# Kernel tuning notes

Hardware: AMD Instinct MI355X
Metric: run time of the kernel (lower is better)

The kernel has to match this reference:

```python
import jax, jax.numpy as jnp
import numpy as np

B, C, H, W = 4, 256, 64, 64
DQK = C // 8  # 32


def setup_inputs() -> dict:
    key = jax.random.key(0)
    ks = jax.random.split(key, 8)
    s = 0.02
    return {
        "x": jax.random.normal(ks[0], (B, C, H, W), dtype=jnp.float32),
        "Wq": jax.random.normal(ks[1], (DQK, C), dtype=jnp.float32) * s,
        "bq": jnp.zeros((DQK,), dtype=jnp.float32),
        "Wk": jax.random.normal(ks[2], (DQK, C), dtype=jnp.float32) * s,
        "bk": jnp.zeros((DQK,), dtype=jnp.float32),
        "Wv": jax.random.normal(ks[3], (C, C), dtype=jnp.float32) * s,
        "bv": jnp.zeros((C,), dtype=jnp.float32),
        "gamma": jax.random.normal(ks[4], (1,), dtype=jnp.float32) * 0.1,
    }


def reference(x, Wq, bq, Wk, bk, Wv, bv, gamma):
    b, c, h, w = x.shape
    n = h * w
    xf = x.reshape(b, c, n)  # [B, C, N]
    # 1x1 convs == per-pixel linear projections
    q = jnp.einsum('dc,bcn->bdn', Wq, xf) + bq[None, :, None]  # [B, C/8, N]
    k = jnp.einsum('dc,bcn->bdn', Wk, xf) + bk[None, :, None]  # [B, C/8, N]
    v = jnp.einsum('dc,bcn->bdn', Wv, xf) + bv[None, :, None]  # [B, C, N]
    # attn[b, i, j] = softmax_j( q_i . k_j / sqrt(C) )
    scores = jnp.einsum('bdn,bdm->bnm', q, k) / (c ** 0.5)  # [B, N, N]
    attn = jax.nn.softmax(scores, axis=-1)
    # out = v @ attn^T : out[b, c, i] = sum_j v[b, c, j] * attn[b, i, j]
    out = jnp.einsum('bcj,bij->bci', v, attn)  # [B, C, N]
    return (gamma * out + xf).reshape(b, c, h, w)
```

## Files before the change

kernel.cpp:

```cpp
#include <hip/hip_runtime.h>

#define NN 4096
#define CC 256
#define DQ 32
#define NB 4

typedef float        f32x4  __attribute__((ext_vector_type(4)));
typedef float        f32x16 __attribute__((ext_vector_type(16)));
typedef short        s16x4  __attribute__((ext_vector_type(4)));
typedef short        s16x8  __attribute__((ext_vector_type(8)));
typedef unsigned int u32x2  __attribute__((ext_vector_type(2)));
typedef unsigned int u32x4  __attribute__((ext_vector_type(4)));

__device__ __forceinline__ unsigned short f2bf(float f) {
  unsigned u = __builtin_bit_cast(unsigned, f);
  u += 0x7fffu + ((u >> 16) & 1u);
  return (unsigned short)(u >> 16);
}

__device__ __forceinline__ f32x4 mfma16(s16x4 a, s16x4 b, f32x4 c) {
  return __builtin_amdgcn_mfma_f32_16x16x16bf16_1k(a, b, c, 0, 0, 0);
}
__device__ __forceinline__ f32x16 mfma32b(s16x8 a, s16x8 b, f32x16 c) {
  return __builtin_amdgcn_mfma_f32_32x32x16_bf16(a, b, c, 0, 0, 0);
}

__device__ __forceinline__ s16x4 lo4(u32x4 r) { u32x2 t = {r[0], r[1]}; return __builtin_bit_cast(s16x4, t); }
__device__ __forceinline__ s16x4 hi4(u32x4 r) { u32x2 t = {r[2], r[3]}; return __builtin_bit_cast(s16x4, t); }
__device__ __forceinline__ s16x8 bc8(u32x4 r) { return __builtin_bit_cast(s16x8, r); }

__device__ __forceinline__ float fexp2(float x) {
  float r;
  asm("v_exp_f32 %0, %1" : "=v"(r) : "v"(x));
  return r;
}

#define XLS 264

__global__ __launch_bounds__(256)
void proj_kernel(const float* __restrict__ x,
                 const float* __restrict__ Wq, const float* __restrict__ bq,
                 const float* __restrict__ Wk, const float* __restrict__ bk,
                 const float* __restrict__ Wv, const float* __restrict__ bv,
                 unsigned short* __restrict__ QT,
                 unsigned short* __restrict__ KT,
                 unsigned short* __restrict__ Vm) {
  __shared__ unsigned short Xl[64 * XLS];
  const int tid = threadIdx.x;
  const int b   = blockIdx.y;
  const int n0  = blockIdx.x * 64;

  {
    const int n4 = (tid & 15) * 4;
    int c = tid >> 4;
    const float* xp = x + (size_t)(b * CC + c) * NN + n0 + n4;
    #pragma unroll
    for (int it = 0; it < 16; ++it) {
      f32x4 v = *reinterpret_cast<const f32x4*>(xp);
      #pragma unroll
      for (int e = 0; e < 4; ++e)
        Xl[(n4 + e) * XLS + c] = f2bf(v[e]);
      c += 16; xp += (size_t)16 * NN;
    }
  }
  __syncthreads();

  const int wave = tid >> 6;
  const int lane = tid & 63;
  const int l16  = lane & 15;
  const int g    = lane >> 4;
  const float qscale = 0.0901684400555602f;

  const float* wrowp[5];
  float wsc[5];
  #pragma unroll
  for (int rt = 0; rt < 5; ++rt) {
    const int R0 = (wave * 5 + rt) * 16;
    const int R  = R0 + l16;
    if (R0 < 32)      { wrowp[rt] = Wq + R * CC;        wsc[rt] = qscale; }
    else if (R0 < 64) { wrowp[rt] = Wk + (R - 32) * CC; wsc[rt] = 1.0f; }
    else              { wrowp[rt] = Wv + (R - 64) * CC; wsc[rt] = 1.0f; }
  }

  f32x4 acc[5][4];
  #pragma unroll
  for (int rt = 0; rt < 5; ++rt)
    #pragma unroll
    for (int nt = 0; nt < 4; ++nt) acc[rt][nt] = (f32x4){0.f, 0.f, 0.f, 0.f};

  for (int k0 = 0; k0 < CC; k0 += 32) {
    s16x4 xb[4][2];
    #pragma unroll
    for (int nt = 0; nt < 4; ++nt) {
      const unsigned short* p = &Xl[(l16 + 16 * nt) * XLS + k0 + 8 * g];
      u32x4 raw = *reinterpret_cast<const u32x4*>(p);
      xb[nt][0] = lo4(raw);
      xb[nt][1] = hi4(raw);
    }
    #pragma unroll
    for (int rt = 0; rt < 5; ++rt) {
      const float* wp = wrowp[rt] + k0 + 8 * g;
      f32x4 w0 = *reinterpret_cast<const f32x4*>(wp);
      f32x4 w1 = *reinterpret_cast<const f32x4*>(wp + 4);
      const float sc = wsc[rt];
      s16x4 wa0, wa1;
      #pragma unroll
      for (int e = 0; e < 4; ++e) {
        wa0[e] = (short)f2bf(w0[e] * sc);
        wa1[e] = (short)f2bf(w1[e] * sc);
      }
      #pragma unroll
      for (int nt = 0; nt < 4; ++nt) {
        acc[rt][nt] = mfma16(wa0, xb[nt][0], acc[rt][nt]);
        acc[rt][nt] = mfma16(wa1, xb[nt][1], acc[rt][nt]);
      }
    }
  }

  #pragma unroll
  for (int rt = 0; rt < 5; ++rt) {
    const int R0 = (wave * 5 + rt) * 16;
    float bias_r[4];
    {
      const float* bp; float bsc;
      if (R0 < 32)      { bp = bq + R0;      bsc = qscale; }
      else if (R0 < 64) { bp = bk + R0 - 32; bsc = 1.0f; }
      else              { bp = bv + R0 - 64; bsc = 1.0f; }
      #pragma unroll
      for (int r = 0; r < 4; ++r) bias_r[r] = bp[4 * g + r] * bsc;
    }
    #pragma unroll
    for (int nt = 0; nt < 4; ++nt) {
      const int n = n0 + nt * 16 + l16;
      float v0 = acc[rt][nt][0] + bias_r[0];
      float v1 = acc[rt][nt][1] + bias_r[1];
      float v2 = acc[rt][nt][2] + bias_r[2];
      float v3 = acc[rt][nt][3] + bias_r[3];
      if (R0 < 32) {
        u32x2 pk = { (unsigned)f2bf(v0) | ((unsigned)f2bf(v1) << 16),
                     (unsigned)f2bf(v2) | ((unsigned)f2bf(v3) << 16) };
        unsigned short* dst = QT + ((size_t)b * NN + n) * DQ + R0 + 4 * g;
        *reinterpret_cast<u32x2*>(dst) = pk;
      } else if (R0 < 64) {
        const int d0     = R0 - 32 + 4 * g;
        const int kh     = d0 >> 4;
        const int g2v    = (d0 >> 3) & 1;
        const int e0     = d0 & 7;
        const int jt     = n >> 5;
        const int lane_t = (n & 31) + 32 * g2v;
        u32x2 pk = { (unsigned)f2bf(v0) | ((unsigned)f2bf(v1) << 16),
                     (unsigned)f2bf(v2) | ((unsigned)f2bf(v3) << 16) };
        unsigned short* kd = KT + (((size_t)(b * 128 + jt) * 2 + kh) * 64 + lane_t) * 8 + e0;
        *reinterpret_cast<u32x2*>(kd) = pk;
      } else {
        const int c0  = R0 - 64 + 4 * g;
        const int cq  = c0 >> 5;
        const int cl  = c0 & 31;
        const int jt  = (n0 + nt * 16) >> 5;
        const int kh  = nt & 1;
        const int g2v = (l16 >> 2) & 1;
        const int e   = (l16 & 3) | (((l16 >> 3) & 1) << 2);
        unsigned short* vd = Vm
          + ((((size_t)(b * 128 + jt) * 8 + cq) * 2 + kh) * 64 + (cl + 32 * g2v)) * 8 + e;
        vd[0]  = f2bf(v0);
        vd[8]  = f2bf(v1);
        vd[16] = f2bf(v2);
        vd[24] = f2bf(v3);
      }
    }
  }
}


#define SM16(SS, L, P0_, P1_) { \
  const float p0=fexp2(SS[0]),  p1=fexp2(SS[1]),  p2=fexp2(SS[2]),  p3=fexp2(SS[3]); \
  const float p4=fexp2(SS[4]),  p5=fexp2(SS[5]),  p6=fexp2(SS[6]),  p7=fexp2(SS[7]); \
  const float p8=fexp2(SS[8]),  p9=fexp2(SS[9]),  pa=fexp2(SS[10]), pb=fexp2(SS[11]); \
  const float pc=fexp2(SS[12]), pd=fexp2(SS[13]), pe=fexp2(SS[14]), pf=fexp2(SS[15]); \
  L += (((p0+p1)+(p2+p3)) + ((p4+p5)+(p6+p7))) + (((p8+p9)+(pa+pb)) + ((pc+pd)+(pe+pf))); \
  unsigned q0,q1,q2,q3,q4,q5,q6,q7; \
  asm("v_cvt_pk_bf16_f32 %0, %1, %2" : "=v"(q0) : "v"(p0), "v"(p1)); \
  asm("v_cvt_pk_bf16_f32 %0, %1, %2" : "=v"(q1) : "v"(p2), "v"(p3)); \
  asm("v_cvt_pk_bf16_f32 %0, %1, %2" : "=v"(q2) : "v"(p4), "v"(p5)); \
  asm("v_cvt_pk_bf16_f32 %0, %1, %2" : "=v"(q3) : "v"(p6), "v"(p7)); \
  asm("v_cvt_pk_bf16_f32 %0, %1, %2" : "=v"(q4) : "v"(p8), "v"(p9)); \
  asm("v_cvt_pk_bf16_f32 %0, %1, %2" : "=v"(q5) : "v"(pa), "v"(pb)); \
  asm("v_cvt_pk_bf16_f32 %0, %1, %2" : "=v"(q6) : "v"(pc), "v"(pd)); \
  asm("v_cvt_pk_bf16_f32 %0, %1, %2" : "=v"(q7) : "v"(pe), "v"(pf)); \
  u32x4 _w0 = {q0,q1,q2,q3}, _w1 = {q4,q5,q6,q7}; \
  P0_ = bc8(_w0); P1_ = bc8(_w1); }

#define LOADK_IMPL(T, KA, KB) { \
  const int _tk = ((T) < 64) ? (T) : 63; \
  const size_t _o = (size_t)_tk * 1024; \
  KA = *(const u32x4*)(Kb + _o); \
  KB = *(const u32x4*)(Kb + _o + 512); }

#define LOADV_IMPL(T, V0, V1, V2, V3) { \
  const int _tv = ((T) < 64) ? (T) : 63; \
  const size_t _o = (size_t)_tv * 8192; \
  V0 = *(const u32x4*)(Vb + _o); \
  V1 = *(const u32x4*)(Vb + _o + 512); \
  V2 = *(const u32x4*)(Vb + _o + 1024); \
  V3 = *(const u32x4*)(Vb + _o + 1536); }

#define ITER_IMPL(T, KA, KB, V0, V1, V2, V3, NKA, NKB, NV0, NV1, NV2, NV3) { \
  LOADK_IMPL((T) + 1, NKA, NKB); \
  LOADV_IMPL((T) + 1, NV0, NV1, NV2, NV3); \
  f32x16 ss = mfma32b(bc8(KA), qf0, zz16); \
  ss = mfma32b(bc8(KB), qf1, ss); \
  s16x8 P0, P1; \
  SM16(ss, l, P0, P1); \
  o0 = mfma32b(bc8(V0), P0, o0); \
  o0 = mfma32b(bc8(V1), P1, o0); \
  o1 = mfma32b(bc8(V2), P0, o1); \
  o1 = mfma32b(bc8(V3), P1, o1); \
}
#define ITER(T, SETC, SETN) ITER_IMPL(T, SETC, SETN)

#define SET_A kA0, kB0, va0, va1, va2, va3
#define SET_B kA1, kB1, vb0, vb1, vb2, vb3

#define PUBLISH_CT(CT, OV) { \
  _Pragma("unroll") \
  for (int r = 0; r < 16; ++r) \
    fb[((cs * 2 + (CT)) * 16 + r) * 64 + lane] = OV[r]; }

#define FINAL_CT(CT, OV) { \
  _Pragma("unroll") \
  for (int r = 0; r < 16; ++r) { \
    const float oB = fb[((cs * 2 + (CT)) * 16 + r) * 64 + lane]; \
    const int   c  = cs * 64 + (CT) * 32 + (r & 3) + 8 * (r >> 2) + 4 * g2; \
    const size_t adr = ((size_t)b * CC + c) * NN + i; \
    out[adr] = ga * (OV[r] + oB) + x[adr]; } }

__global__ __launch_bounds__(512)
void attn_kernel(const unsigned short* __restrict__ QT,
                 const unsigned short* __restrict__ KT,
                 const unsigned short* __restrict__ Vm,
                 const float* __restrict__ x,
                 const float* __restrict__ gamma,
                 float* __restrict__ out) {
  __shared__ float fb[8192 + 32];

  const int tid  = threadIdx.x;
  const int wave = tid >> 6;
  const int jq   = wave >> 2;
  const int cs   = wave & 3;
  const int lane = tid & 63;
  const int l31  = lane & 31;
  const int g2   = lane >> 5;

  const int gid = blockIdx.x;
  const int rr  = gid & 7;
  const int qq  = gid >> 3;
  const int b   = rr >> 1;
  const int xt  = (qq << 1) | (rr & 1);
  const int ibase = xt * 32;
  const float gamma0 = gamma[0];

  const unsigned short* Qb = QT + ((size_t)b * NN + ibase + l31) * DQ;
  const s16x8 qf0 = bc8(*(const u32x4*)(Qb + 8 * g2));
  const s16x8 qf1 = bc8(*(const u32x4*)(Qb + 16 + 8 * g2));

  f32x16 o0, o1, zz16;
  #pragma unroll
  for (int r = 0; r < 16; ++r) { o0[r] = 0.f; o1[r] = 0.f; zz16[r] = 0.f; }
  float l = 0.f;

  const unsigned short* Kb = KT + (size_t)(b * 128 + jq * 64) * 1024 + lane * 8;
  const unsigned short* Vb = Vm + ((size_t)(b * 128 + jq * 64) * 8 + cs * 2) * 1024 + lane * 8;

  u32x4 kA0, kB0, va0, va1, va2, va3;
  u32x4 kA1, kB1, vb0, vb1, vb2, vb3;

  LOADK_IMPL(0, kA0, kB0);
  LOADV_IMPL(0, va0, va1, va2, va3);

  #pragma unroll 1
  for (int tt = 0; tt < 32; ++tt) {
    const int t = 2 * tt;
    ITER(t,     SET_A, SET_B);
    ITER(t + 1, SET_B, SET_A);
  }

  l += __shfl_xor(l, 32);

  if (jq == 1) {
    PUBLISH_CT(0, o0);
    PUBLISH_CT(1, o1);
    if (cs == 0 && g2 == 0) fb[8192 + l31] = l;
  }
  __syncthreads();
  if (jq == 0) {
    const float lB = fb[8192 + l31];
    const float ga = gamma0 / (l + lB);
    const int i = ibase + l31;
    FINAL_CT(0, o0);
    FINAL_CT(1, o1);
  }
}

extern "C" void kernel_launch(void* const* d_in, const int* in_sizes, int n_in,
                              void* d_out, int out_size, void* d_ws, size_t ws_size,
                              hipStream_t stream) {
  const float* x     = (const float*)d_in[0];
  const float* Wq    = (const float*)d_in[1];
  const float* bq    = (const float*)d_in[2];
  const float* Wk    = (const float*)d_in[3];
  const float* bk    = (const float*)d_in[4];
  const float* Wv    = (const float*)d_in[5];
  const float* bv    = (const float*)d_in[6];
  const float* gamma = (const float*)d_in[7];
  float* out = (float*)d_out;

  unsigned short* QT = (unsigned short*)d_ws;
  unsigned short* KT = QT + (size_t)NB * NN * DQ;
  unsigned short* Vm = KT + (size_t)NB * NN * DQ;

  dim3 gridP(64, NB), blkP(256);
  proj_kernel<<<gridP, blkP, 0, stream>>>(x, Wq, bq, Wk, bk, Wv, bv, QT, KT, Vm);
  attn_kernel<<<512, 512, 0, stream>>>(QT, KT, Vm, x, gamma, out);
}
```

Before: 86.21 us.

## Split key range four ways per block, widen channel slice per wave

Work inside each 512-thread block is repartitioned. Waves now split the key dimension into four quarters and the channel dimension into two halves of 128 channels, where before it was two key halves and four 64-channel slices. Each wave therefore recomputes fewer redundant QK scores and softmax exponentials (2 channel groups instead of 4 redo the same scores) while doing more PV MFMAs per score. In exchange each wave holds twice as many accumulator and V-prefetch registers, which may lower occupancy. The partial results go through a two-stage LDS reduction with an extra barrier, using 64KB of dynamic shared memory.

Result: no change. 85.02 us (-1.4%).

```diff
diff --git a/kernel.cpp b/kernel.cpp
--- a/kernel.cpp
+++ b/kernel.cpp
@@ -191,22 +191,27 @@
   P0_ = bc8(_w0); P1_ = bc8(_w1); }
 
 #define LOADK_IMPL(T, KA, KB) { \
-  const int _tk = ((T) < 64) ? (T) : 63; \
+  const int _tk = ((T) < 32) ? (T) : 31; \
   const size_t _o = (size_t)_tk * 1024; \
   KA = *(const u32x4*)(Kb + _o); \
   KB = *(const u32x4*)(Kb + _o + 512); }
 
-#define LOADV_IMPL(T, V0, V1, V2, V3) { \
-  const int _tv = ((T) < 64) ? (T) : 63; \
+#define LOADV_IMPL(T, V0, V1, V2, V3, V4, V5, V6, V7) { \
+  const int _tv = ((T) < 32) ? (T) : 31; \
   const size_t _o = (size_t)_tv * 8192; \
   V0 = *(const u32x4*)(Vb + _o); \
   V1 = *(const u32x4*)(Vb + _o + 512); \
   V2 = *(const u32x4*)(Vb + _o + 1024); \
-  V3 = *(const u32x4*)(Vb + _o + 1536); }
-
-#define ITER_IMPL(T, KA, KB, V0, V1, V2, V3, NKA, NKB, NV0, NV1, NV2, NV3) { \
+  V3 = *(const u32x4*)(Vb + _o + 1536); \
+  V4 = *(const u32x4*)(Vb + _o + 2048); \
+  V5 = *(const u32x4*)(Vb + _o + 2560); \
+  V6 = *(const u32x4*)(Vb + _o + 3072); \
+  V7 = *(const u32x4*)(Vb + _o + 3584); }
+
+#define ITER_IMPL(T, KA, KB, V0, V1, V2, V3, V4, V5, V6, V7, \
+                     NKA, NKB, NV0, NV1, NV2, NV3, NV4, NV5, NV6, NV7) { \
   LOADK_IMPL((T) + 1, NKA, NKB); \
-  LOADV_IMPL((T) + 1, NV0, NV1, NV2, NV3); \
+  LOADV_IMPL((T) + 1, NV0, NV1, NV2, NV3, NV4, NV5, NV6, NV7); \
   f32x16 ss = mfma32b(bc8(KA), qf0, zz16); \
   ss = mfma32b(bc8(KB), qf1, ss); \
   s16x8 P0, P1; \
@@ -215,22 +220,34 @@
   o0 = mfma32b(bc8(V1), P1, o0); \
   o1 = mfma32b(bc8(V2), P0, o1); \
   o1 = mfma32b(bc8(V3), P1, o1); \
+  o2 = mfma32b(bc8(V4), P0, o2); \
+  o2 = mfma32b(bc8(V5), P1, o2); \
+  o3 = mfma32b(bc8(V6), P0, o3); \
+  o3 = mfma32b(bc8(V7), P1, o3); \
 }
 #define ITER(T, SETC, SETN) ITER_IMPL(T, SETC, SETN)
 
-#define SET_A kA0, kB0, va0, va1, va2, va3
-#define SET_B kA1, kB1, vb0, vb1, vb2, vb3
-
-#define PUBLISH_CT(CT, OV) { \
+#define SET_A kA0, kB0, va0, va1, va2, va3, va4, va5, va6, va7
+#define SET_B kA1, kB1, vb0, vb1, vb2, vb3, vb4, vb5, vb6, vb7
+
+#define S1IDX(CT, R) ((((jq * 2 + cs) * 4 + (CT)) * 16 + (R)) * 64 + lane)
+#define S2IDX(CT, R) (((cs * 4 + (CT)) * 16 + (R)) * 64 + lane)
+#define LOFF 16384
+
+#define PUB1_CT(CT, OV) { \
   _Pragma("unroll") \
-  for (int r = 0; r < 16; ++r) \
-    fb[((cs * 2 + (CT)) * 16 + r) * 64 + lane] = OV[r]; }
-
-#define FINAL_CT(CT, OV) { \
+  for (int r = 0; r < 16; ++r) fb[S1IDX(CT, r)] = OV[r]; }
+#define ABS1_CT(CT, OV) { \
+  _Pragma("unroll") \
+  for (int r = 0; r < 16; ++r) OV[r] += fb[S1IDX(CT, r)]; }
+#define PUB2_CT(CT, OV) { \
+  _Pragma("unroll") \
+  for (int r = 0; r < 16; ++r) fb[S2IDX(CT, r)] = OV[r]; }
+#define FIN_CT(CT, OV) { \
   _Pragma("unroll") \
   for (int r = 0; r < 16; ++r) { \
-    const float oB = fb[((cs * 2 + (CT)) * 16 + r) * 64 + lane]; \
-    const int   c  = cs * 64 + (CT) * 32 + (r & 3) + 8 * (r >> 2) + 4 * g2; \
+    const float oB = fb[S2IDX(CT, r)]; \
+    const int   c  = cs * 128 + (CT) * 32 + (r & 3) + 8 * (r >> 2) + 4 * g2; \
     const size_t adr = ((size_t)b * CC + c) * NN + i; \
     out[adr] = ga * (OV[r] + oB) + x[adr]; } }
 
@@ -241,15 +258,17 @@
                  const float* __restrict__ x,
                  const float* __restrict__ gamma,
                  float* __restrict__ out) {
-  __shared__ float fb[8192 + 32];
+  extern __shared__ float fb[];
 
   const int tid  = threadIdx.x;
   const int wave = tid >> 6;
   const int jq   = wave >> 2;
-  const int cs   = wave & 3;
+  const int jsub = (wave >> 1) & 1;
+  const int cs   = wave & 1;
   const int lane = tid & 63;
   const int l31  = lane & 31;
   const int g2   = lane >> 5;
+  const int jquarter = jq * 2 + jsub;
 
   const int gid = blockIdx.x;
   const int rr  = gid & 7;
@@ -263,22 +282,22 @@
   const s16x8 qf0 = bc8(*(const u32x4*)(Qb + 8 * g2));
   const s16x8 qf1 = bc8(*(const u32x4*)(Qb + 16 + 8 * g2));
 
-  f32x16 o0, o1, zz16;
+  f32x16 o0, o1, o2, o3, zz16;
   #pragma unroll
-  for (int r = 0; r < 16; ++r) { o0[r] = 0.f; o1[r] = 0.f; zz16[r] = 0.f; }
+  for (int r = 0; r < 16; ++r) { o0[r] = 0.f; o1[r] = 0.f; o2[r] = 0.f; o3[r] = 0.f; zz16[r] = 0.f; }
   float l = 0.f;
 
-  const unsigned short* Kb = KT + (size_t)(b * 128 + jq * 64) * 1024 + lane * 8;
-  const unsigned short* Vb = Vm + ((size_t)(b * 128 + jq * 64) * 8 + cs * 2) * 1024 + lane * 8;
-
-  u32x4 kA0, kB0, va0, va1, va2, va3;
-  u32x4 kA1, kB1, vb0, vb1, vb2, vb3;
+  const unsigned short* Kb = KT + (size_t)(b * 128 + jquarter * 32) * 1024 + lane * 8;
+  const unsigned short* Vb = Vm + ((size_t)(b * 128 + jquarter * 32) * 8 + cs * 4) * 1024 + lane * 8;
+
+  u32x4 kA0, kB0, va0, va1, va2, va3, va4, va5, va6, va7;
+  u32x4 kA1, kB1, vb0, vb1, vb2, vb3, vb4, vb5, vb6, vb7;
 
   LOADK_IMPL(0, kA0, kB0);
-  LOADV_IMPL(0, va0, va1, va2, va3);
+  LOADV_IMPL(0, va0, va1, va2, va3, va4, va5, va6, va7);
 
   #pragma unroll 1
-  for (int tt = 0; tt < 32; ++tt) {
+  for (int tt = 0; tt < 16; ++tt) {
     const int t = 2 * tt;
     ITER(t,     SET_A, SET_B);
     ITER(t + 1, SET_B, SET_A);
@@ -286,18 +305,37 @@
 
   l += __shfl_xor(l, 32);
 
-  if (jq == 1) {
-    PUBLISH_CT(0, o0);
-    PUBLISH_CT(1, o1);
-    if (cs == 0 && g2 == 0) fb[8192 + l31] = l;
+  if (jsub == 1) {
+    PUB1_CT(0, o0);
+    PUB1_CT(1, o1);
+    PUB1_CT(2, o2);
+    PUB1_CT(3, o3);
+    if (cs == 0 && g2 == 0) fb[LOFF + jq * 32 + l31] = l;
   }
   __syncthreads();
-  if (jq == 0) {
-    const float lB = fb[8192 + l31];
+  if (jsub == 0) {
+    ABS1_CT(0, o0);
+    ABS1_CT(1, o1);
+    ABS1_CT(2, o2);
+    ABS1_CT(3, o3);
+    l += fb[LOFF + jq * 32 + l31];
+    if (jq == 1) {
+      PUB2_CT(0, o0);
+      PUB2_CT(1, o1);
+      PUB2_CT(2, o2);
+      PUB2_CT(3, o3);
+      if (cs == 0 && g2 == 0) fb[LOFF + 64 + l31] = l;
+    }
+  }
+  __syncthreads();
+  if (jsub == 0 && jq == 0) {
+    const float lB = fb[LOFF + 64 + l31];
     const float ga = gamma0 / (l + lB);
     const int i = ibase + l31;
-    FINAL_CT(0, o0);
-    FINAL_CT(1, o1);
+    FIN_CT(0, o0);
+    FIN_CT(1, o1);
+    FIN_CT(2, o2);
+    FIN_CT(3, o3);
   }
 }
 
@@ -318,7 +356,15 @@
   unsigned short* KT = QT + (size_t)NB * NN * DQ;
   unsigned short* Vm = KT + (size_t)NB * NN * DQ;
 
+  const int ldsB = (16384 + 128) * 4;
+  static bool attr_set = false;
+  if (!attr_set) {
+    hipFuncSetAttribute((const void*)attn_kernel,
+                        hipFuncAttributeMaxDynamicSharedMemorySize, ldsB);
+    attr_set = true;
+  }
+
   dim3 gridP(64, NB), blkP(256);
   proj_kernel<<<gridP, blkP, 0, stream>>>(x, Wq, bq, Wk, bk, Wv, bv, QT, KT, Vm);
-  attn_kernel<<<512, 512, 0, stream>>>(QT, KT, Vm, x, gamma, out);
-}
+  attn_kernel<<<512, 512, ldsB, stream>>>(QT, KT, Vm, x, gamma, out);
+}
```
